# Optimization experiments

Measured on AMD Instinct MI355X. Metric: run time of the kernel, lower is better.

The kernel has to match this reference:

```python
import jax, jax.numpy as jnp
import numpy as np

B, L, E, H, W = 2, 4096, 512, 8, 128
D = E // H

def _clin(x, Wr, Wi, br, bi):
    # ComplexLinear on real input: out = x@(Wr + i*Wi)^T + (br + i*bi)
    return x @ Wr.T + br, x @ Wi.T + bi

def setup_inputs() -> dict:
    key = jax.random.key(0)
    ks = jax.random.split(key, 20)
    s = 0.02
    d = {
        'query': jax.random.normal(ks[0], (B, L, E), jnp.float32),
        'key':   jax.random.normal(ks[1], (B, L, E), jnp.float32),
        'value': jax.random.normal(ks[2], (B, L, E), jnp.float32),
    }
    names = ['q', 'k', 'v', 'o']
    i = 3
    for n in names:
        d[n + 'Wr'] = jax.random.normal(ks[i], (E, E), jnp.float32) * s; i += 1
        d[n + 'Wi'] = jax.random.normal(ks[i], (E, E), jnp.float32) * s; i += 1
        d[n + 'br'] = jnp.zeros((E,), jnp.float32)
        d[n + 'bi'] = jnp.zeros((E,), jnp.float32)
    return d

def reference(query, key, value,
              qWr, qWi, qbr, qbi,
              kWr, kWi, kbr, kbi,
              vWr, vWi, vbr, vbi,
              oWr, oWi, obr, obi):
    # complex projections (real input -> complex output, kept as (re, im) float pairs)
    qr, qi = _clin(query, qWr, qWi, qbr, qbi)
    kr, ki = _clin(key,   kWr, kWi, kbr, kbi)
    vr, _vi = _clin(value, vWr, vWi, vbr, vbi)  # imag part of V is discarded by the real cast

    def heads(x):
        return x.reshape(B, L, H, D).transpose(0, 2, 1, 3)  # [B,H,L,D]
    qr, qi, kr, ki, vr = map(heads, (qr, qi, kr, ki, vr))

    # Re(q @ k^H) = qr@kr^T + qi@ki^T  (only the real part is ever used)
    scale = 1.0 / np.sqrt(D)
    scores = (jnp.einsum('bhld,bhmd->bhlm', qr, kr)
              + jnp.einsum('bhld,bhmd->bhlm', qi, ki)) * scale

    # Faithful to source: only lower_mask is applied (window_mask is built but never added).
    idx = jnp.arange(L)
    lower_mask = jnp.where(idx[:, None] - idx[None, :] >= W + 1,
                           -jnp.inf, 0.0).astype(scores.dtype)
    probs = jax.nn.softmax(scores + lower_mask, axis=-1)

    # out = probs @ v; cast to query.dtype keeps only Re = probs @ vr
    o = jnp.einsum('bhlm,bhmd->bhld', probs, vr)
    o = o.transpose(0, 2, 1, 3).reshape(B, L, E)

    out_r = o @ oWr.T + obr
    out_i = o @ oWi.T + obi
    return out_r, out_i
```

## Files before the change

### kernel.cpp

```cpp
#include <hip/hip_runtime.h>


typedef unsigned short u16;
typedef unsigned int u32;
typedef __attribute__((ext_vector_type(8))) short bf16x8;
typedef __attribute__((ext_vector_type(4))) float f32x4;
typedef __attribute__((ext_vector_type(16))) float f32x16;
typedef __attribute__((ext_vector_type(4))) u32 u32x4;

#define L_ 4096
#define E_ 512
#define M_ 8192

__device__ __forceinline__ u16 f2bf(float f) {
  union { float f; u32 u; } v; v.f = f;
  return (u16)((v.u + 0x7FFFu + ((v.u >> 16) & 1u)) >> 16);
}

__device__ __forceinline__ void gll16(const void* g, void* l) {
  __builtin_amdgcn_global_load_lds(
      (const __attribute__((address_space(1))) u32*)g,
      (__attribute__((address_space(3))) u32*)l, 16, 0, 0);
}

__global__ void cvt_x_kernel(const float* __restrict__ q, const float* __restrict__ k,
                             const float* __restrict__ v,
                             u16* __restrict__ xq, u16* __restrict__ xk, u16* __restrict__ xv) {
  const int total = 3 * (M_ * E_ / 4);
  int stride = gridDim.x * blockDim.x;
  for (int u = blockIdx.x * blockDim.x + threadIdx.x; u < total; u += stride) {
    int mat = u >> 20, e = u & ((1 << 20) - 1);
    const float4 f = ((const float4*)(mat == 0 ? q : mat == 1 ? k : v))[e];
    ushort4 o = make_ushort4(f2bf(f.x), f2bf(f.y), f2bf(f.z), f2bf(f.w));
    *(ushort4*)((mat == 0 ? xq : mat == 1 ? xk : xv) + (size_t)e * 4) = o;
  }
}

struct CPtrs { const float* w[7]; const float* b[7]; };

__global__ void cvt_wb_kernel(CPtrs p, u16* __restrict__ wcat, float* __restrict__ bcat) {
  const int total = 7 * (E_ * E_ / 4);
  int stride = gridDim.x * blockDim.x;
  int t0 = blockIdx.x * blockDim.x + threadIdx.x;
  for (int u = t0; u < total; u += stride) {
    int wi = u >> 16, e = u & 65535;
    const float4 f = ((const float4*)p.w[wi])[e];
    ushort4 o = make_ushort4(f2bf(f.x), f2bf(f.y), f2bf(f.z), f2bf(f.w));
    *(ushort4*)(wcat + (size_t)wi * 262144 + (size_t)e * 4) = o;
  }
  for (int j = t0; j < 3584; j += stride) bcat[j] = p.b[j >> 9][j & 511];
}

__device__ __forceinline__ void gemm128_main(const u16* __restrict__ A, const u16* __restrict__ Bw,
                                             int m0, int n0w, char* sm, f32x4 acc[4][4]) {
  int tid = threadIdx.x;
  int lane = tid & 63, w = tid >> 6;
  int wm = w >> 1, wn = w & 1;
#pragma unroll
  for (int a = 0; a < 4; a++)
#pragma unroll
    for (int b = 0; b < 4; b++)
#pragma unroll
      for (int j = 0; j < 4; j++) acc[a][b][j] = 0.f;

  auto stage = [&](int buf, int ks) {
    char* dst = sm + buf * 16384;
#pragma unroll
    for (int n = 0; n < 2; n++) {
      int u = n * 256 + tid;
      int row = u >> 2, c = u & 3;
      int so = (c ^ (row & 3)) * 16;
      int ldso = (n * 256 + w * 64) * 16;
      gll16((const char*)(A + (size_t)(m0 + row) * 512 + ks * 32) + so, dst + ldso);
      gll16((const char*)(Bw + (size_t)(n0w + row) * 512 + ks * 32) + so, dst + 8192 + ldso);
    }
  };

  stage(0, 0);
  __syncthreads();
  int cur = 0;
  for (int ks = 0; ks < 16; ks++) {
    if (ks < 15) stage(cur ^ 1, ks + 1);
    const char* as = sm + cur * 16384;
    const char* bs = as + 8192;
    bf16x8 af[4], bfr[4];
#pragma unroll
    for (int i = 0; i < 4; i++) {
      int ra = wm * 64 + i * 16 + (lane & 15);
      af[i] = *(const bf16x8*)(as + ra * 64 + (((lane >> 4) * 16) ^ ((ra & 3) << 4)));
      int rb = wn * 64 + i * 16 + (lane & 15);
      bfr[i] = *(const bf16x8*)(bs + rb * 64 + (((lane >> 4) * 16) ^ ((rb & 3) << 4)));
    }
    __builtin_amdgcn_s_setprio(1);
#pragma unroll
    for (int mt = 0; mt < 4; mt++)
#pragma unroll
      for (int nt = 0; nt < 4; nt++)
        acc[mt][nt] = __builtin_amdgcn_mfma_f32_16x16x32_bf16(af[mt], bfr[nt], acc[mt][nt], 0, 0, 0);
    __builtin_amdgcn_s_setprio(0);
    __syncthreads();
    cur ^= 1;
  }
}

__global__ __launch_bounds__(256) void proj_kernel(
    const u16* __restrict__ xq, const u16* __restrict__ xk, const u16* __restrict__ xv,
    const u16* __restrict__ wcat, const float* __restrict__ bcat,
    u16* __restrict__ qrb, u16* __restrict__ qib,
    u16* __restrict__ krb, u16* __restrict__ kib, u16* __restrict__ vtb) {
  __shared__ alignas(16) char sm[32768];
  int bx = blockIdx.x, by = blockIdx.y;
  const u16* A = bx < 8 ? xq : (bx < 16 ? xk : xv);
  int m0 = by * 128, n0w = bx * 128;
  f32x4 acc[4][4];
  gemm128_main(A, wcat, m0, n0w, sm, acc);

  int lane = threadIdx.x & 63, w = threadIdx.x >> 6;
  int wm = w >> 1, wn = w & 1;
  int lL = lane & 15, lH = lane >> 4;
#pragma unroll
  for (int mt = 0; mt < 4; mt++) {
#pragma unroll
    for (int nt = 0; nt < 4; nt++) {
      int n = n0w + wn * 64 + nt * 16 + lL;
      float bias = bcat[n];
      int e = n & 511;
#pragma unroll
      for (int j = 0; j < 4; j++) {
        int m = m0 + wm * 64 + mt * 16 + lH * 4 + j;
        float val = acc[mt][nt][j] + bias;
        int bb = m >> 12, ll = m & 4095;
        if (bx < 16) {
          if (bx < 8) val *= 0.18033688011112042f;
          u16* dst = (bx < 8) ? ((n & 512) ? qib : qrb) : ((n & 512) ? kib : krb);
          dst[((size_t)((bb * 8 + (e >> 6)) * 4096 + ll) << 6) + (e & 63)] = f2bf(val);
        } else {
          vtb[((size_t)((bb * 8 + (e >> 6)) * 64 + (e & 63)) << 12) + ll] = f2bf(val);
        }
      }
    }
  }
}

__global__ __launch_bounds__(256) void oproj_kernel(
    const u16* __restrict__ obf, const u16* __restrict__ wcat, const float* __restrict__ bcat,
    float* __restrict__ out) {
  __shared__ alignas(16) char sm[32768];
  int bx = blockIdx.x, by = blockIdx.y;
  int m0 = by * 128, n0w = 2560 + bx * 128;
  f32x4 acc[4][4];
  gemm128_main(obf, wcat, m0, n0w, sm, acc);

  int lane = threadIdx.x & 63, w = threadIdx.x >> 6;
  int wm = w >> 1, wn = w & 1;
  int lL = lane & 15, lH = lane >> 4;
#pragma unroll
  for (int mt = 0; mt < 4; mt++) {
#pragma unroll
    for (int nt = 0; nt < 4; nt++) {
      int n = n0w + wn * 64 + nt * 16 + lL;
      float bias = bcat[n];
      int nn = n - 2560;
      float* dst = out + ((nn & 512) ? 4194304 : 0) + (nn & 511);
#pragma unroll
      for (int j = 0; j < 4; j++) {
        int m = m0 + wm * 64 + mt * 16 + lH * 4 + j;
        dst[(size_t)m * 512] = acc[mt][nt][j] + bias;
      }
    }
  }
}

__global__ __launch_bounds__(256, 2) void attn_kernel(
    const u16* __restrict__ qrb, const u16* __restrict__ qib,
    const u16* __restrict__ krb, const u16* __restrict__ kib,
    const u16* __restrict__ vtb, u16* __restrict__ obf) {
  __shared__ alignas(16) char sm[3 * 24576];
  int bid = blockIdx.x;
  int bh = bid & 15;
  int q2 = bid >> 4;
  int qt = (q2 < 16) ? q2 : (47 - q2);
  int bb = bh >> 3, hh = bh & 7;
  int i0 = qt << 7;
  int tid = threadIdx.x;
  int lane = tid & 63, w = tid >> 6;
  int lo = lane & 31, hi = lane >> 5;
  int i0w = i0 + w * 32;
  int irow = i0w + lo;

  bf16x8 fqr[4], fqi[4];
  {
    const u16* qp = qrb + ((size_t)(bh * 4096 + irow) << 6) + hi * 8;
    const u16* qip = qib + ((size_t)(bh * 4096 + irow) << 6) + hi * 8;
#pragma unroll
    for (int c = 0; c < 4; c++) {
      fqr[c] = *(const bf16x8*)(qp + c * 16);
      fqi[c] = *(const bf16x8*)(qip + c * 16);
    }
  }

  f32x16 oa0, oa1;
#pragma unroll
  for (int r = 0; r < 16; r++) { oa0[r] = 0.f; oa1[r] = 0.f; }
  float l_run = 0.f;

  int jstart = (i0 >= 128) ? (i0 - 128) : 0;
  int ntiles = (4096 - jstart) >> 6;

  auto stage = [&](char* dst, int j0) {
#pragma unroll
    for (int n = 0; n < 2; n++) {
      int u = n * 256 + tid;
      int row = u >> 3, c = u & 7;
      int so = (c ^ (row & 7)) * 16;
      int ldso = (n * 256 + w * 64) * 16;
      size_t krow = ((size_t)(bh * 4096 + j0 + row) << 6);
      gll16((const char*)(krb + krow) + so, dst + ldso);
      gll16((const char*)(kib + krow) + so, dst + 8192 + ldso);
      size_t vrow = ((size_t)(bh * 64 + row) << 12) + j0;
      gll16((const char*)(vtb + vrow) + so, dst + 16384 + ldso);
    }
  };

  int swz = (lo & 7) << 4;

  auto qk = [&](const char* Kbase, f32x16& s0, f32x16& s1) {
    const char* Kr = Kbase;
    const char* Ki = Kbase + 8192;
#pragma unroll
    for (int r = 0; r < 16; r++) { s0[r] = 0.f; s1[r] = 0.f; }
#pragma unroll
    for (int c = 0; c < 4; c++) {
      int off = (c * 32 + hi * 16) ^ swz;
      bf16x8 a0r = *(const bf16x8*)(Kr + lo * 128 + off);
      bf16x8 a0i = *(const bf16x8*)(Ki + lo * 128 + off);
      bf16x8 a1r = *(const bf16x8*)(Kr + (32 + lo) * 128 + off);
      bf16x8 a1i = *(const bf16x8*)(Ki + (32 + lo) * 128 + off);
      __builtin_amdgcn_s_setprio(1);
      s0 = __builtin_amdgcn_mfma_f32_32x32x16_bf16(a0r, fqr[c], s0, 0, 0, 0);
      s1 = __builtin_amdgcn_mfma_f32_32x32x16_bf16(a1r, fqr[c], s1, 0, 0, 0);
      s0 = __builtin_amdgcn_mfma_f32_32x32x16_bf16(a0i, fqi[c], s0, 0, 0, 0);
      s1 = __builtin_amdgcn_mfma_f32_32x32x16_bf16(a1i, fqi[c], s1, 0, 0, 0);
      __builtin_amdgcn_s_setprio(0);
    }
  };

  auto cvtpk = [](float a, float b) -> u32 {
    u32 r;
    asm("v_cvt_pk_bf16_f32 %0, %1, %2" : "=v"(r) : "v"(a), "v"(b));
    return r;
  };
  auto mkfrag = [&](const float* p, bf16x8& fA, bf16x8& fB) {
    u32 x0 = cvtpk(p[0], p[1]), y0 = cvtpk(p[4], p[5]);
    u32 x1 = cvtpk(p[2], p[3]), y1 = cvtpk(p[6], p[7]);
    u32 x2 = cvtpk(p[8], p[9]), y2 = cvtpk(p[12], p[13]);
    u32 x3 = cvtpk(p[10], p[11]), y3 = cvtpk(p[14], p[15]);
    asm("v_permlane32_swap_b32 %0, %1" : "+v"(x0), "+v"(y0));
    asm("v_permlane32_swap_b32 %0, %1" : "+v"(x1), "+v"(y1));
    asm("v_permlane32_swap_b32 %0, %1" : "+v"(x2), "+v"(y2));
    asm("v_permlane32_swap_b32 %0, %1" : "+v"(x3), "+v"(y3));
    u32x4 a; a[0] = x0; a[1] = x1; a[2] = y0; a[3] = y1;
    u32x4 b; b[0] = x2; b[1] = x3; b[2] = y2; b[3] = y3;
    fA = __builtin_bit_cast(bf16x8, a);
    fB = __builtin_bit_cast(bf16x8, b);
  };

  auto smpv = [&](const char* Kbase, int j0, f32x16& s0, f32x16& s1) {
    if (j0 <= i0w - 98) {
#pragma unroll
      for (int r = 0; r < 16; r++) {
        int kk = j0 + (r & 3) + ((r >> 2) << 3) + (hi << 2);
        if (kk <= irow - 129) s0[r] = -3e38f;
        if (kk + 32 <= irow - 129) s1[r] = -3e38f;
      }
    }

    float ps0 = 0.f, ps1 = 0.f, ps2 = 0.f, ps3 = 0.f;
#pragma unroll
    for (int r = 0; r < 16; r += 4) {
      s0[r] = exp2f(s0[r]);     ps0 += s0[r];
      s0[r + 1] = exp2f(s0[r + 1]); ps1 += s0[r + 1];
      s0[r + 2] = exp2f(s0[r + 2]); ps2 += s0[r + 2];
      s0[r + 3] = exp2f(s0[r + 3]); ps3 += s0[r + 3];
    }
#pragma unroll
    for (int r = 0; r < 16; r += 4) {
      s1[r] = exp2f(s1[r]);     ps0 += s1[r];
      s1[r + 1] = exp2f(s1[r + 1]); ps1 += s1[r + 1];
      s1[r + 2] = exp2f(s1[r + 2]); ps2 += s1[r + 2];
      s1[r + 3] = exp2f(s1[r + 3]); ps3 += s1[r + 3];
    }
    float psum = (ps0 + ps1) + (ps2 + ps3);
    psum += __shfl_xor(psum, 32);
    l_run += psum;

    bf16x8 pf0, pf1, pf2, pf3;
    mkfrag((const float*)&s0, pf0, pf1);
    mkfrag((const float*)&s1, pf2, pf3);

    const char* Vt = Kbase + 16384;
#pragma unroll
    for (int kc = 0; kc < 4; kc++) {
      int off = (kc * 32 + hi * 16) ^ swz;
      bf16x8 av0 = *(const bf16x8*)(Vt + lo * 128 + off);
      bf16x8 av1 = *(const bf16x8*)(Vt + (32 + lo) * 128 + off);
      bf16x8 pk = (kc == 0) ? pf0 : (kc == 1) ? pf1 : (kc == 2) ? pf2 : pf3;
      __builtin_amdgcn_s_setprio(1);
      oa0 = __builtin_amdgcn_mfma_f32_32x32x16_bf16(av0, pk, oa0, 0, 0, 0);
      oa1 = __builtin_amdgcn_mfma_f32_32x32x16_bf16(av1, pk, oa1, 0, 0, 0);
      __builtin_amdgcn_s_setprio(0);
    }
  };

  char* cur = sm;
  char* nxt = sm + 24576;
  char* nx2 = sm + 49152;

  stage(cur, jstart);
  stage(nxt, jstart + 64);
  __syncthreads();

  f32x16 sA0, sA1, sB0, sB1;
  qk(cur, sA0, sA1);

  for (int t = 0; t < ntiles; t += 2) {
    int j0 = jstart + (t << 6);
    if (t + 2 < ntiles) stage(nx2, j0 + 128);
    qk(nxt, sB0, sB1);
    smpv(cur, j0, sA0, sA1);
    __syncthreads();
    { char* tmp = cur; cur = nxt; nxt = nx2; nx2 = tmp; }
    if (t + 3 < ntiles) stage(nx2, j0 + 192);
    if (t + 2 < ntiles) qk(nxt, sA0, sA1);
    smpv(cur, j0 + 64, sB0, sB1);
    __syncthreads();
    { char* tmp = cur; cur = nxt; nxt = nx2; nx2 = tmp; }
  }

  float rl = 1.0f / l_run;
  u16* orow = obf + ((size_t)(bb * 4096 + irow) << 9) + hh * 64;
#pragma unroll
  for (int g = 0; g < 4; g++) {
    ushort4 v0 = make_ushort4(f2bf(oa0[4 * g] * rl), f2bf(oa0[4 * g + 1] * rl),
                              f2bf(oa0[4 * g + 2] * rl), f2bf(oa0[4 * g + 3] * rl));
    *(ushort4*)(orow + g * 8 + hi * 4) = v0;
    ushort4 v1 = make_ushort4(f2bf(oa1[4 * g] * rl), f2bf(oa1[4 * g + 1] * rl),
                              f2bf(oa1[4 * g + 2] * rl), f2bf(oa1[4 * g + 3] * rl));
    *(ushort4*)(orow + 32 + g * 8 + hi * 4) = v1;
  }
}

extern "C" void kernel_launch(void* const* d_in, const int* in_sizes, int n_in,
                              void* d_out, int out_size, void* d_ws, size_t ws_size,
                              hipStream_t stream) {
  (void)in_sizes; (void)n_in; (void)out_size; (void)ws_size;
  const float* q = (const float*)d_in[0];
  const float* k = (const float*)d_in[1];
  const float* v = (const float*)d_in[2];
  char* ws = (char*)d_ws;
  u16* wcat = (u16*)(ws + 0x000000);
  float* bcat = (float*)(ws + 0x400000);
  u16* xq  = (u16*)(ws + 0x500000);
  u16* xk  = (u16*)(ws + 0xD00000);
  u16* xv  = (u16*)(ws + 0x1500000);
  u16* qrb = (u16*)(ws + 0x1D00000);
  u16* qib = (u16*)(ws + 0x2500000);
  u16* krb = (u16*)(ws + 0x2D00000);
  u16* kib = (u16*)(ws + 0x3500000);
  u16* vtb = (u16*)(ws + 0x3D00000);
  u16* obf = xq;
  float* out = (float*)d_out;

  cvt_x_kernel<<<2048, 256, 0, stream>>>(q, k, v, xq, xk, xv);

  CPtrs cp;
  cp.w[0] = (const float*)d_in[3];  cp.w[1] = (const float*)d_in[4];
  cp.w[2] = (const float*)d_in[7];  cp.w[3] = (const float*)d_in[8];
  cp.w[4] = (const float*)d_in[11]; cp.w[5] = (const float*)d_in[15]; cp.w[6] = (const float*)d_in[16];
  cp.b[0] = (const float*)d_in[5];  cp.b[1] = (const float*)d_in[6];
  cp.b[2] = (const float*)d_in[9];  cp.b[3] = (const float*)d_in[10];
  cp.b[4] = (const float*)d_in[13]; cp.b[5] = (const float*)d_in[17]; cp.b[6] = (const float*)d_in[18];
  cvt_wb_kernel<<<448, 256, 0, stream>>>(cp, wcat, bcat);

  proj_kernel<<<dim3(20, 64), 256, 0, stream>>>(xq, xk, xv, wcat, bcat, qrb, qib, krb, kib, vtb);
  attn_kernel<<<512, 256, 0, stream>>>(qrb, qib, krb, kib, vtb, obf);
  oproj_kernel<<<dim3(8, 64), 256, 0, stream>>>(obf, wcat, bcat, out);
}
```

Before: 184.9 us.

## Split attention key range across two wave groups with LDS merge of partial outputs

The attention kernel now launches 512 threads per block, with two groups of four waves. Each group processes alternating 32-key sub-tiles of every 64-key chunk, so each wave does half the QK and PV MFMA work per iteration. Staging uses precomputed per-thread global pointers that advance each step, on a 3-slot ring. At the end, group 1 writes its partial output accumulators and row sums to LDS, and group 0 merges them and writes the normalized result. This doubles the waves available to hide latency, at the cost of a final LDS reduction, more registers per block, and a tighter occupancy target of 4 waves per SIMD.

```diff
diff --git a/kernel.cpp b/kernel.cpp
--- a/kernel.cpp
+++ b/kernel.cpp
@@ -171,11 +171,11 @@
   }
 }
 
-__global__ __launch_bounds__(256, 2) void attn_kernel(
+__global__ __launch_bounds__(512, 4) void attn_kernel(
     const u16* __restrict__ qrb, const u16* __restrict__ qib,
     const u16* __restrict__ krb, const u16* __restrict__ kib,
     const u16* __restrict__ vtb, u16* __restrict__ obf) {
-  __shared__ alignas(16) char sm[3 * 24576];
+  __shared__ alignas(16) char sm[73728];
   int bid = blockIdx.x;
   int bh = bid & 15;
   int q2 = bid >> 4;
@@ -184,9 +184,14 @@
   int i0 = qt << 7;
   int tid = threadIdx.x;
   int lane = tid & 63, w = tid >> 6;
+  int grp = w >> 2, wq = w & 3;
   int lo = lane & 31, hi = lane >> 5;
-  int i0w = i0 + w * 32;
+  int i0w = i0 + wq * 32;
   int irow = i0w + lo;
+
+  int jstart = (i0 >= 128) ? (i0 - 128) : 0;
+  int ntiles = (4096 - jstart) >> 5;
+  int nper = ntiles >> 1;
 
   bf16x8 fqr[4], fqi[4];
   {
@@ -199,154 +204,165 @@
     }
   }
 
-  f32x16 oa0, oa1;
-#pragma unroll
-  for (int r = 0; r < 16; r++) { oa0[r] = 0.f; oa1[r] = 0.f; }
-  float l_run = 0.f;
-
-  int jstart = (i0 >= 128) ? (i0 - 128) : 0;
-  int ntiles = (4096 - jstart) >> 6;
-
-  auto stage = [&](char* dst, int j0) {
-#pragma unroll
-    for (int n = 0; n < 2; n++) {
-      int u = n * 256 + tid;
-      int row = u >> 3, c = u & 7;
-      int so = (c ^ (row & 7)) * 16;
-      int ldso = (n * 256 + w * 64) * 16;
-      size_t krow = ((size_t)(bh * 4096 + j0 + row) << 6);
-      gll16((const char*)(krb + krow) + so, dst + ldso);
-      gll16((const char*)(kib + krow) + so, dst + 8192 + ldso);
-      size_t vrow = ((size_t)(bh * 64 + row) << 12) + j0;
-      gll16((const char*)(vtb + vrow) + so, dst + 16384 + ldso);
+  const char* gp[3];
+  int adv[3], ldso[3];
+  {
+    const char* krbB = (const char*)krb + ((size_t)(bh * 4096 + jstart) << 7);
+    const char* kibB = (const char*)kib + ((size_t)(bh * 4096 + jstart) << 7);
+    const char* vtbB = (const char*)vtb + ((size_t)(bh * 64) << 13) + ((size_t)jstart << 1);
+    int tI = grp;
+#pragma unroll
+    for (int s = 0; s < 3; s++) {
+      int cc = 3 * w + s;
+      int c12 = cc - 12 * tI;
+      ldso[s] = cc * 1024;
+      if (c12 < 8) {
+        int r = (c12 & 3) * 8 + (lane >> 3);
+        int so = ((lane & 7) ^ (r & 7)) << 4;
+        gp[s] = (c12 < 4 ? krbB : kibB) + (size_t)(tI * 32 + r) * 128 + so;
+        adv[s] = 8192;
+      } else {
+        int dr = (c12 - 8) * 16 + (lane >> 2);
+        int so = ((lane & 3) ^ (dr & 3)) << 4;
+        gp[s] = vtbB + (size_t)dr * 8192 + tI * 64 + so;
+        adv[s] = 128;
+      }
+    }
+  }
+  auto stagep = [&](char* sb) {
+#pragma unroll
+    for (int s = 0; s < 3; s++) {
+      gll16(gp[s], sb + ldso[s]);
+      gp[s] += adv[s];
     }
   };
 
-  int swz = (lo & 7) << 4;
-
-  auto qk = [&](const char* Kbase, f32x16& s0, f32x16& s1) {
-    const char* Kr = Kbase;
-    const char* Ki = Kbase + 8192;
-#pragma unroll
-    for (int r = 0; r < 16; r++) { s0[r] = 0.f; s1[r] = 0.f; }
-#pragma unroll
-    for (int c = 0; c < 4; c++) {
-      int off = (c * 32 + hi * 16) ^ swz;
-      bf16x8 a0r = *(const bf16x8*)(Kr + lo * 128 + off);
-      bf16x8 a0i = *(const bf16x8*)(Ki + lo * 128 + off);
-      bf16x8 a1r = *(const bf16x8*)(Kr + (32 + lo) * 128 + off);
-      bf16x8 a1i = *(const bf16x8*)(Ki + (32 + lo) * 128 + off);
-      __builtin_amdgcn_s_setprio(1);
-      s0 = __builtin_amdgcn_mfma_f32_32x32x16_bf16(a0r, fqr[c], s0, 0, 0, 0);
-      s1 = __builtin_amdgcn_mfma_f32_32x32x16_bf16(a1r, fqr[c], s1, 0, 0, 0);
-      s0 = __builtin_amdgcn_mfma_f32_32x32x16_bf16(a0i, fqi[c], s0, 0, 0, 0);
-      s1 = __builtin_amdgcn_mfma_f32_32x32x16_bf16(a1i, fqi[c], s1, 0, 0, 0);
-      __builtin_amdgcn_s_setprio(0);
-    }
-  };
+  int offK[4], offV[2];
+#pragma unroll
+  for (int c = 0; c < 4; c++) offK[c] = lo * 128 + ((c * 32 + hi * 16) ^ ((lo & 7) << 4));
+#pragma unroll
+  for (int kc = 0; kc < 2; kc++) offV[kc] = 8192 + lo * 64 + ((kc * 32 + hi * 16) ^ ((lo & 3) << 4));
 
   auto cvtpk = [](float a, float b) -> u32 {
     u32 r;
     asm("v_cvt_pk_bf16_f32 %0, %1, %2" : "=v"(r) : "v"(a), "v"(b));
     return r;
   };
-  auto mkfrag = [&](const float* p, bf16x8& fA, bf16x8& fB) {
-    u32 x0 = cvtpk(p[0], p[1]), y0 = cvtpk(p[4], p[5]);
-    u32 x1 = cvtpk(p[2], p[3]), y1 = cvtpk(p[6], p[7]);
-    u32 x2 = cvtpk(p[8], p[9]), y2 = cvtpk(p[12], p[13]);
-    u32 x3 = cvtpk(p[10], p[11]), y3 = cvtpk(p[14], p[15]);
-    asm("v_permlane32_swap_b32 %0, %1" : "+v"(x0), "+v"(y0));
-    asm("v_permlane32_swap_b32 %0, %1" : "+v"(x1), "+v"(y1));
-    asm("v_permlane32_swap_b32 %0, %1" : "+v"(x2), "+v"(y2));
-    asm("v_permlane32_swap_b32 %0, %1" : "+v"(x3), "+v"(y3));
-    u32x4 a; a[0] = x0; a[1] = x1; a[2] = y0; a[3] = y1;
-    u32x4 b; b[0] = x2; b[1] = x3; b[2] = y2; b[3] = y3;
-    fA = __builtin_bit_cast(bf16x8, a);
-    fB = __builtin_bit_cast(bf16x8, b);
-  };
-
-  auto smpv = [&](const char* Kbase, int j0, f32x16& s0, f32x16& s1) {
+
+  f32x16 oa0, oa1;
+#pragma unroll
+  for (int r = 0; r < 16; r++) { oa0[r] = 0.f; oa1[r] = 0.f; }
+  float l_run = 0.f;
+  const int iband = irow - 129;
+
+  stagep(sm);
+  __syncthreads();
+  char* rb = sm + grp * 12288;
+  char* sb = sm + 24576;
+  int j0 = jstart + grp * 32;
+
+  for (int p = 0; p < nper; p++) {
+    if (p + 1 < nper) {
+      stagep(sb);
+      sb += 24576; if (sb == sm + 73728) sb = sm;
+    }
+    f32x16 s0;
+#pragma unroll
+    for (int r = 0; r < 16; r++) s0[r] = 0.f;
+#pragma unroll
+    for (int c = 0; c < 4; c++) {
+      bf16x8 ar = *(const bf16x8*)(rb + offK[c]);
+      bf16x8 ai = *(const bf16x8*)(rb + 4096 + offK[c]);
+      __builtin_amdgcn_s_setprio(1);
+      s0 = __builtin_amdgcn_mfma_f32_32x32x16_bf16(ar, fqr[c], s0, 0, 0, 0);
+      s0 = __builtin_amdgcn_mfma_f32_32x32x16_bf16(ai, fqi[c], s0, 0, 0, 0);
+      __builtin_amdgcn_s_setprio(0);
+    }
     if (j0 <= i0w - 98) {
 #pragma unroll
       for (int r = 0; r < 16; r++) {
         int kk = j0 + (r & 3) + ((r >> 2) << 3) + (hi << 2);
-        if (kk <= irow - 129) s0[r] = -3e38f;
-        if (kk + 32 <= irow - 129) s1[r] = -3e38f;
+        if (kk <= iband) s0[r] = -3e38f;
       }
     }
-
     float ps0 = 0.f, ps1 = 0.f, ps2 = 0.f, ps3 = 0.f;
 #pragma unroll
     for (int r = 0; r < 16; r += 4) {
-      s0[r] = exp2f(s0[r]);     ps0 += s0[r];
+      s0[r] = exp2f(s0[r]);         ps0 += s0[r];
       s0[r + 1] = exp2f(s0[r + 1]); ps1 += s0[r + 1];
       s0[r + 2] = exp2f(s0[r + 2]); ps2 += s0[r + 2];
       s0[r + 3] = exp2f(s0[r + 3]); ps3 += s0[r + 3];
     }
-#pragma unroll
-    for (int r = 0; r < 16; r += 4) {
-      s1[r] = exp2f(s1[r]);     ps0 += s1[r];
-      s1[r + 1] = exp2f(s1[r + 1]); ps1 += s1[r + 1];
-      s1[r + 2] = exp2f(s1[r + 2]); ps2 += s1[r + 2];
-      s1[r + 3] = exp2f(s1[r + 3]); ps3 += s1[r + 3];
-    }
     float psum = (ps0 + ps1) + (ps2 + ps3);
     psum += __shfl_xor(psum, 32);
     l_run += psum;
 
-    bf16x8 pf0, pf1, pf2, pf3;
-    mkfrag((const float*)&s0, pf0, pf1);
-    mkfrag((const float*)&s1, pf2, pf3);
-
-    const char* Vt = Kbase + 16384;
-#pragma unroll
-    for (int kc = 0; kc < 4; kc++) {
-      int off = (kc * 32 + hi * 16) ^ swz;
-      bf16x8 av0 = *(const bf16x8*)(Vt + lo * 128 + off);
-      bf16x8 av1 = *(const bf16x8*)(Vt + (32 + lo) * 128 + off);
-      bf16x8 pk = (kc == 0) ? pf0 : (kc == 1) ? pf1 : (kc == 2) ? pf2 : pf3;
+    bf16x8 pf0, pf1;
+    {
+      const float* pp = (const float*)&s0;
+      u32 x0 = cvtpk(pp[0], pp[1]), y0 = cvtpk(pp[4], pp[5]);
+      u32 x1 = cvtpk(pp[2], pp[3]), y1 = cvtpk(pp[6], pp[7]);
+      u32 x2 = cvtpk(pp[8], pp[9]), y2 = cvtpk(pp[12], pp[13]);
+      u32 x3 = cvtpk(pp[10], pp[11]), y3 = cvtpk(pp[14], pp[15]);
+      asm("v_permlane32_swap_b32 %0, %1" : "+v"(x0), "+v"(y0));
+      asm("v_permlane32_swap_b32 %0, %1" : "+v"(x1), "+v"(y1));
+      asm("v_permlane32_swap_b32 %0, %1" : "+v"(x2), "+v"(y2));
+      asm("v_permlane32_swap_b32 %0, %1" : "+v"(x3), "+v"(y3));
+      u32x4 a; a[0] = x0; a[1] = x1; a[2] = y0; a[3] = y1;
+      u32x4 b; b[0] = x2; b[1] = x3; b[2] = y2; b[3] = y3;
+      pf0 = __builtin_bit_cast(bf16x8, a);
+      pf1 = __builtin_bit_cast(bf16x8, b);
+    }
+    {
+      bf16x8 av00 = *(const bf16x8*)(rb + offV[0]);
+      bf16x8 av01 = *(const bf16x8*)(rb + offV[0] + 2048);
+      bf16x8 av10 = *(const bf16x8*)(rb + offV[1]);
+      bf16x8 av11 = *(const bf16x8*)(rb + offV[1] + 2048);
       __builtin_amdgcn_s_setprio(1);
-      oa0 = __builtin_amdgcn_mfma_f32_32x32x16_bf16(av0, pk, oa0, 0, 0, 0);
-      oa1 = __builtin_amdgcn_mfma_f32_32x32x16_bf16(av1, pk, oa1, 0, 0, 0);
+      oa0 = __builtin_amdgcn_mfma_f32_32x32x16_bf16(av00, pf0, oa0, 0, 0, 0);
+      oa1 = __builtin_amdgcn_mfma_f32_32x32x16_bf16(av01, pf0, oa1, 0, 0, 0);
+      oa0 = __builtin_amdgcn_mfma_f32_32x32x16_bf16(av10, pf1, oa0, 0, 0, 0);
+      oa1 = __builtin_amdgcn_mfma_f32_32x32x16_bf16(av11, pf1, oa1, 0, 0, 0);
       __builtin_amdgcn_s_setprio(0);
     }
-  };
-
-  char* cur = sm;
-  char* nxt = sm + 24576;
-  char* nx2 = sm + 49152;
-
-  stage(cur, jstart);
-  stage(nxt, jstart + 64);
+    rb += 24576; if (rb >= sm + 73728) rb -= 73728;
+    j0 += 64;
+    __syncthreads();
+  }
+
+  int swo = (lo & 7) << 4;
+  char* ob = sm + wq * 8192;
+  if (grp == 1) {
+#pragma unroll
+    for (int g2 = 0; g2 < 4; g2++) {
+      f32x4 v0; f32x4 v1;
+#pragma unroll
+      for (int e = 0; e < 4; e++) { v0[e] = oa0[4 * g2 + e]; v1[e] = oa1[4 * g2 + e]; }
+      *(f32x4*)(ob + lo * 256 + ((g2 * 32 + hi * 16) ^ swo)) = v0;
+      *(f32x4*)(ob + lo * 256 + ((128 + g2 * 32 + hi * 16) ^ swo)) = v1;
+    }
+    if (!hi) *(float*)(sm + 32768 + wq * 128 + lo * 4) = l_run;
+  }
   __syncthreads();
-
-  f32x16 sA0, sA1, sB0, sB1;
-  qk(cur, sA0, sA1);
-
-  for (int t = 0; t < ntiles; t += 2) {
-    int j0 = jstart + (t << 6);
-    if (t + 2 < ntiles) stage(nx2, j0 + 128);
-    qk(nxt, sB0, sB1);
-    smpv(cur, j0, sA0, sA1);
-    __syncthreads();
-    { char* tmp = cur; cur = nxt; nxt = nx2; nx2 = tmp; }
-    if (t + 3 < ntiles) stage(nx2, j0 + 192);
-    if (t + 2 < ntiles) qk(nxt, sA0, sA1);
-    smpv(cur, j0 + 64, sB0, sB1);
-    __syncthreads();
-    { char* tmp = cur; cur = nxt; nxt = nx2; nx2 = tmp; }
-  }
-
-  float rl = 1.0f / l_run;
-  u16* orow = obf + ((size_t)(bb * 4096 + irow) << 9) + hh * 64;
-#pragma unroll
-  for (int g = 0; g < 4; g++) {
-    ushort4 v0 = make_ushort4(f2bf(oa0[4 * g] * rl), f2bf(oa0[4 * g + 1] * rl),
-                              f2bf(oa0[4 * g + 2] * rl), f2bf(oa0[4 * g + 3] * rl));
-    *(ushort4*)(orow + g * 8 + hi * 4) = v0;
-    ushort4 v1 = make_ushort4(f2bf(oa1[4 * g] * rl), f2bf(oa1[4 * g + 1] * rl),
-                              f2bf(oa1[4 * g + 2] * rl), f2bf(oa1[4 * g + 3] * rl));
-    *(ushort4*)(orow + 32 + g * 8 + hi * 4) = v1;
+  if (grp == 0) {
+    float l2 = *(const float*)(sm + 32768 + wq * 128 + lo * 4);
+    float rl = 1.0f / (l_run + l2);
+    u16* orow = obf + ((size_t)(bb * 4096 + irow) << 9) + hh * 64;
+#pragma unroll
+    for (int g2 = 0; g2 < 4; g2++) {
+      f32x4 v0 = *(const f32x4*)(ob + lo * 256 + ((g2 * 32 + hi * 16) ^ swo));
+      f32x4 v1 = *(const f32x4*)(ob + lo * 256 + ((128 + g2 * 32 + hi * 16) ^ swo));
+      ushort4 o0 = make_ushort4(f2bf((oa0[4 * g2] + v0[0]) * rl),
+                                f2bf((oa0[4 * g2 + 1] + v0[1]) * rl),
+                                f2bf((oa0[4 * g2 + 2] + v0[2]) * rl),
+                                f2bf((oa0[4 * g2 + 3] + v0[3]) * rl));
+      *(ushort4*)(orow + g2 * 8 + hi * 4) = o0;
+      ushort4 o1 = make_ushort4(f2bf((oa1[4 * g2] + v1[0]) * rl),
+                                f2bf((oa1[4 * g2 + 1] + v1[1]) * rl),
+                                f2bf((oa1[4 * g2 + 2] + v1[2]) * rl),
+                                f2bf((oa1[4 * g2 + 3] + v1[3]) * rl));
+      *(ushort4*)(orow + 32 + g2 * 8 + hi * 4) = o1;
+    }
   }
 }
 
@@ -383,6 +399,6 @@
   cvt_wb_kernel<<<448, 256, 0, stream>>>(cp, wcat, bcat);
 
   proj_kernel<<<dim3(20, 64), 256, 0, stream>>>(xq, xk, xv, wcat, bcat, qrb, qib, krb, kib, vtb);
-  attn_kernel<<<512, 256, 0, stream>>>(qrb, qib, krb, kib, vtb, obf);
+  attn_kernel<<<512, 512, 0, stream>>>(qrb, qib, krb, kib, vtb, obf);
   oproj_kernel<<<dim3(8, 64), 256, 0, stream>>>(obf, wcat, bcat, out);
 }
```

Result: faster. 174.8 us (-5.5%).
